# Kernel tuning notes

Measured on AMD Instinct MI355X. Metric: run time of the kernel, lower is better.

Reference implementation:

```python
import jax, jax.numpy as jnp
import numpy as np

B, N_ANGLES, LR, LZ = 1, 120, 128, 192
PAD = int(np.ceil(LR * (np.sqrt(2.0) - 1.0) / 2.0))  # pad_image amount = 27
LP = LR + 2 * PAD                                     # padded plane size = 182
DELTA = 1e-11


def _rotate_plane(vol, phi):
    """Bilinear CCW rotation by phi (radians) of the (dim1, dim2) plane of
    vol [B, L, L, Z] about its center, zero fill outside (grid_sample-style)."""
    L = vol.shape[1]
    c = (L - 1) / 2.0
    g = jnp.arange(L, dtype=jnp.float32) - c
    y, x = jnp.meshgrid(g, g, indexing='ij')          # [L, L]
    cp, sp = jnp.cos(phi), jnp.sin(phi)
    sy = cp * y - sp * x + c                          # source coords (inverse map)
    sx = sp * y + cp * x + c
    y0 = jnp.floor(sy)
    x0 = jnp.floor(sx)
    wy = (sy - y0)[None, :, :, None]
    wx = (sx - x0)[None, :, :, None]
    y0i = y0.astype(jnp.int32)
    x0i = x0.astype(jnp.int32)

    def tap(yi, xi):
        valid = ((yi >= 0) & (yi < L) & (xi >= 0) & (xi < L)).astype(vol.dtype)
        v = vol[:, jnp.clip(yi, 0, L - 1), jnp.clip(xi, 0, L - 1), :]  # [B,L,L,Z]
        return v * valid[None, :, :, None]

    return ((1 - wy) * (1 - wx) * tap(y0i, x0i)
            + (1 - wy) * wx * tap(y0i, x0i + 1)
            + wy * (1 - wx) * tap(y0i + 1, x0i)
            + wy * wx * tap(y0i + 1, x0i + 1))


def _back_project(image):
    # image: [B, N_angles, Lr, Lz]
    img_p = jnp.pad(image, ((0, 0), (0, 0), (PAD, PAD), (0, 0)))   # pad_image along Lr
    slices = jnp.transpose(img_p, (1, 0, 2, 3))                     # [N, B, LP, LZ]
    angles = jnp.arange(N_ANGLES, dtype=jnp.float32) * (2.0 * jnp.pi / N_ANGLES)
    phis = 1.5 * jnp.pi - angles   # rotate_detector_z(..., negative=True): +(270deg - angle)
    ones2d = jnp.ones((1, LP, LP, 1), image.dtype)

    def body(carry, inp):
        obj, norm2d = carry
        sl, phi = inp                                               # sl: [B, LP, LZ]
        vol = jnp.broadcast_to(sl[:, None, :, :], (sl.shape[0], LP, LP, sl.shape[2]))
        rot = _rotate_plane(vol, phi)                               # [B, LP, LP, LZ]
        obj = obj + rot[:, PAD:PAD + LR, PAD:PAD + LR, :]           # unpad_object
        # norm_constant_i is all-ones, constant over batch and z -> track 2D pattern
        w = _rotate_plane(ones2d, phi)[0, PAD:PAD + LR, PAD:PAD + LR, 0]
        return (obj, norm2d + w), None

    init = (jnp.zeros((image.shape[0], LR, LR, LZ), image.dtype),
            jnp.zeros((LR, LR), image.dtype))
    (obj, norm2d), _ = jax.lax.scan(body, init, (slices, phis))
    return obj / (norm2d[None, :, :, None] + DELTA)


def setup_inputs() -> dict:
    key = jax.random.key(0)
    image = jax.random.uniform(key, (B, N_ANGLES, LR, LZ), dtype=jnp.float32)
    return {"image": image}


def reference(image):
    return _back_project(image)
```

## Files before the change

### kernel.cpp

```cpp
#include <hip/hip_runtime.h>
#include <math.h>

namespace {

constexpr int NA = 120;
constexpr int LR = 128;
constexpr int LZ = 192;
constexpr int UW2 = 182;
constexpr int ZSTR = UW2 * 16;
constexpr int ASTR = 24 * ZSTR;
constexpr float CTR = 63.5f;

typedef float v2f __attribute__((ext_vector_type(2)));
typedef _Float16 half_t;
typedef half_t v2h __attribute__((ext_vector_type(2)));

#if defined(__has_builtin)
#if __has_builtin(__builtin_amdgcn_cvt_pk_f16_fp8) && __has_builtin(__builtin_amdgcn_fdot2)
#define USE_F16_DOT 1
#endif
#endif

__device__ inline void pk_fma(v2f& acc, v2f w, v2f t) {
    asm("v_pk_fma_f32 %0, %1, %2, %0" : "+v"(acc) : "v"(w), "v"(t));
}

__global__ __launch_bounds__(256) void cvt9(const float* __restrict__ img,
                                            unsigned char* __restrict__ pb) {
    const int idx = blockIdx.x * 256 + threadIdx.x;
    if (idx >= NA * UW2 * 24) return;
    const int up = idx % UW2;
    const int t  = idx / UW2;
    const int zb = t % 24;
    const int a  = t / 24;
    const int z0 = zb * 8;
    const int r0 = up - 27;
    const int r1 = up - 26;

    float v0[8], v1[8];
    if (r0 >= 0 && r0 < LR) {
        const float4* p = reinterpret_cast<const float4*>(img + (a * LR + r0) * LZ + z0);
        const float4 x = p[0], y = p[1];
        v0[0]=x.x; v0[1]=x.y; v0[2]=x.z; v0[3]=x.w;
        v0[4]=y.x; v0[5]=y.y; v0[6]=y.z; v0[7]=y.w;
    } else {
#pragma unroll
        for (int j = 0; j < 8; ++j) v0[j] = 0.f;
    }
    if (r1 >= 0 && r1 < LR) {
        const float4* p = reinterpret_cast<const float4*>(img + (a * LR + r1) * LZ + z0);
        const float4 x = p[0], y = p[1];
        v1[0]=x.x; v1[1]=x.y; v1[2]=x.z; v1[3]=x.w;
        v1[4]=y.x; v1[5]=y.y; v1[6]=y.z; v1[7]=y.w;
    } else {
#pragma unroll
        for (int j = 0; j < 8; ++j) v1[j] = 0.f;
    }

    uint4 o;
    unsigned* od = &o.x;
#pragma unroll
    for (int d = 0; d < 4; ++d) {
        int w = __builtin_amdgcn_cvt_pk_fp8_f32(v0[2*d]   - 0.5f, v1[2*d]   - 0.5f, 0, false);
        w = __builtin_amdgcn_cvt_pk_fp8_f32(v0[2*d+1] - 0.5f, v1[2*d+1] - 0.5f, w, true);
        od[d] = (unsigned)w;
    }
    *reinterpret_cast<uint4*>(pb + ((size_t)a * ASTR + (size_t)zb * ZSTR + (size_t)up * 16)) = o;
}

struct __align__(8) G13 {
    unsigned w;
    unsigned boff;
};

__global__ __launch_bounds__(384, 6) void bp_v13(const unsigned char* __restrict__ pb,
                                                 float* __restrict__ out) {
    __shared__ float2 s_cs[NA];
    __shared__ G13 s_geo[NA + 4][16];

    const int tid = threadIdx.x;

    if (tid < NA) {
        const float ang = (float)tid * (float)(2.0 * M_PI / (double)NA);
        const float phi = (float)(1.5 * M_PI) - ang;
        s_cs[tid] = make_float2(cosf(phi), sinf(phi));
    }
    __syncthreads();

    const int bid = blockIdx.x;
    const int swz = (bid & 7) * 128 + (bid >> 3);
    const int y  = swz >> 3;
    const int xg = (swz & 7) << 4;

    const float Y = (float)y - CTR;
    for (int e = tid; e < 16 * (NA + 4); e += 384) {
        const int p = e & 15;
        const int t = e >> 4;
        G13 g;
        if (t < NA) {
            const float2 cs = s_cs[t];
            const float X = (float)(xg + p) - CTR;
            const float u  = fmaf(cs.y, Y, fmaf(cs.x, X, CTR));
            const float fl = floorf(u);
            const float wx = u - fl;
#ifdef USE_F16_DOT
            union { v2h h; unsigned u32; } cw;
            cw.h = (v2h){(half_t)(1.0f - wx), (half_t)wx};
            g.w = cw.u32;
#else
            g.w = __float_as_uint(1.0f - wx);
#endif
            g.boff = (unsigned)(t * ASTR + ((int)fl + 27) * 16);
        } else {
            g.w = 0u; g.boff = 0;
        }
        s_geo[t][p] = g;
    }
    __syncthreads();

    const int px = tid & 15;
    const int zo = tid >> 4;
    const unsigned zbase = (unsigned)(zo * ZSTR);

#ifdef USE_F16_DOT
    float fac[8];
#pragma unroll
    for (int j = 0; j < 8; ++j) fac[j] = 0.f;
#else
    v2f acc[8];
#pragma unroll
    for (int j = 0; j < 8; ++j) acc[j] = (v2f){0.f, 0.f};
#endif

    unsigned wr[4];
    uint4 T[4];
#pragma unroll
    for (int k = 0; k < 4; ++k) {
        const G13 g = s_geo[k][px];
        wr[k] = g.w;
        T[k] = *reinterpret_cast<const uint4*>(pb + (g.boff + zbase));
    }

    for (int t0 = 0; t0 < NA; t0 += 4) {
#pragma unroll
        for (int k = 0; k < 4; ++k) {
            const uint4 cur = T[k];
            const unsigned cwb = wr[k];
            const G13 g = s_geo[t0 + k + 4][px];
            wr[k] = g.w;
            T[k] = *reinterpret_cast<const uint4*>(pb + (g.boff + zbase));
            const unsigned* q = &cur.x;
#ifdef USE_F16_DOT
            union { unsigned u32; v2h h; } cw;
            cw.u32 = cwb;
#pragma unroll
            for (int d = 0; d < 4; ++d) {
                const v2h lo = __builtin_amdgcn_cvt_pk_f16_fp8((short)(q[d] & 0xffffu));
                const v2h hi = __builtin_amdgcn_cvt_pk_f16_fp8((short)(q[d] >> 16));
                fac[2*d + 0] = __builtin_amdgcn_fdot2(cw.h, lo, fac[2*d + 0], false);
                fac[2*d + 1] = __builtin_amdgcn_fdot2(cw.h, hi, fac[2*d + 1], false);
            }
#else
            const float cw0 = __uint_as_float(cwb);
            const v2f cw = {cw0, 1.0f - cw0};
#pragma unroll
            for (int d = 0; d < 4; ++d) {
                const v2f lo = __builtin_amdgcn_cvt_pk_f32_fp8((int)q[d], false);
                const v2f hi = __builtin_amdgcn_cvt_pk_f32_fp8((int)q[d], true);
                pk_fma(acc[2*d + 0], cw, lo);
                pk_fma(acc[2*d + 1], cw, hi);
            }
#endif
        }
    }

    const float inv = (float)(1.0 / (120.0 + 1e-11));
    float* op = out + (size_t)(y * LR + xg + px) * LZ + zo * 8;
    float4 r0, r1;
#ifdef USE_F16_DOT
    r0.x = (fac[0] + 60.0f) * inv;
    r0.y = (fac[1] + 60.0f) * inv;
    r0.z = (fac[2] + 60.0f) * inv;
    r0.w = (fac[3] + 60.0f) * inv;
    r1.x = (fac[4] + 60.0f) * inv;
    r1.y = (fac[5] + 60.0f) * inv;
    r1.z = (fac[6] + 60.0f) * inv;
    r1.w = (fac[7] + 60.0f) * inv;
#else
    r0.x = (acc[0][0] + acc[0][1] + 60.0f) * inv;
    r0.y = (acc[1][0] + acc[1][1] + 60.0f) * inv;
    r0.z = (acc[2][0] + acc[2][1] + 60.0f) * inv;
    r0.w = (acc[3][0] + acc[3][1] + 60.0f) * inv;
    r1.x = (acc[4][0] + acc[4][1] + 60.0f) * inv;
    r1.y = (acc[5][0] + acc[5][1] + 60.0f) * inv;
    r1.z = (acc[6][0] + acc[6][1] + 60.0f) * inv;
    r1.w = (acc[7][0] + acc[7][1] + 60.0f) * inv;
#endif
    *reinterpret_cast<float4*>(op)     = r0;
    *reinterpret_cast<float4*>(op + 4) = r1;
}

struct __align__(16) Geo {
    float w0, w1;
    int b0, b1;
};

__global__ __launch_bounds__(256) void cvt_fp8(const float* __restrict__ in,
                                               unsigned int* __restrict__ out8,
                                               int n16) {
    const int i = blockIdx.x * 256 + threadIdx.x;
    if (i >= n16) return;
    const float4* p = reinterpret_cast<const float4*>(in) + (size_t)i * 4;
    uint4 o;
    unsigned int* od = &o.x;
#pragma unroll
    for (int d = 0; d < 4; ++d) {
        const float4 f = p[d];
        int w = __builtin_amdgcn_cvt_pk_fp8_f32(f.x - 0.5f, f.y - 0.5f, 0, false);
        w = __builtin_amdgcn_cvt_pk_fp8_f32(f.z - 0.5f, f.w - 0.5f, w, true);
        od[d] = (unsigned int)w;
    }
    reinterpret_cast<uint4*>(out8)[i] = o;
}

__device__ inline void blend8(v2f acc[4], float w0, float w1,
                              const uint2& t0, const uint2& t1) {
    const v2f W0 = {w0, w0};
    const v2f W1 = {w1, w1};
    const unsigned int* q0 = &t0.x;
    const unsigned int* q1 = &t1.x;
#pragma unroll
    for (int d = 0; d < 2; ++d) {
        const v2f a_lo = __builtin_amdgcn_cvt_pk_f32_fp8((int)q0[d], false);
        const v2f a_hi = __builtin_amdgcn_cvt_pk_f32_fp8((int)q0[d], true);
        const v2f b_lo = __builtin_amdgcn_cvt_pk_f32_fp8((int)q1[d], false);
        const v2f b_hi = __builtin_amdgcn_cvt_pk_f32_fp8((int)q1[d], true);
        acc[2 * d + 0] = acc[2 * d + 0] + W0 * a_lo + W1 * b_lo;
        acc[2 * d + 1] = acc[2 * d + 1] + W0 * a_hi + W1 * b_hi;
    }
}

__global__ __launch_bounds__(192, 6) void bp_v5(const unsigned char* __restrict__ img,
                                                float* __restrict__ out) {
    __shared__ float2 s_cs[NA];
    __shared__ Geo s_geo[NA][8];
    __shared__ float s_sumw[8];

    const int tid = threadIdx.x;
    if (tid < NA) {
        const float ang = (float)tid * (float)(2.0 * M_PI / (double)NA);
        const float phi = (float)(1.5 * M_PI) - ang;
        s_cs[tid] = make_float2(cosf(phi), sinf(phi));
    }
    __syncthreads();

    const int bid = blockIdx.x;
    const int swz = (bid & 7) * 256 + (bid >> 3);
    const int y  = swz >> 4;
    const int xg = (swz & 15) << 3;

    const float Y = (float)y - CTR;
    for (int e = tid; e < 8 * NA; e += 192) {
        const int p = e & 7;
        const int a = e >> 3;
        const float2 cs = s_cs[a];
        const float X = (float)(xg + p) - CTR;
        const float u  = fmaf(cs.y, Y, fmaf(cs.x, X, CTR));
        const float fl = floorf(u);
        const float wx = u - fl;
        const int i0 = (int)fl;
        Geo g;
        g.w0 = ((unsigned)i0 < 128u) ? (1.0f - wx) : 0.0f;
        g.w1 = ((unsigned)(i0 + 1) < 128u) ? wx : 0.0f;
        const int o0 = min(max(i0, 0), LR - 1);
        const int o1 = min(max(i0 + 1, 0), LR - 1);
        g.b0 = (a * LR + o0) * LZ;
        g.b1 = (a * LR + o1) * LZ;
        s_geo[a][p] = g;
    }
    __syncthreads();

    if (tid < 8) {
        float s = 0.f;
        for (int a = 0; a < NA; ++a) s += s_geo[a][tid].w0 + s_geo[a][tid].w1;
        s_sumw[tid] = s;
    }
    __syncthreads();

    const int zo = tid % 24;
    const int px = tid / 24;
    const unsigned char* base = img + zo * 8;

    v2f acc[4];
#pragma unroll
    for (int j = 0; j < 4; ++j) acc[j] = (v2f){0.f, 0.f};

    Geo ga = s_geo[0][px];
    Geo gb = s_geo[1][px];
    uint2 A0 = *reinterpret_cast<const uint2*>(base + ga.b0);
    uint2 A1 = *reinterpret_cast<const uint2*>(base + ga.b1);
    uint2 B0 = *reinterpret_cast<const uint2*>(base + gb.b0);
    uint2 B1 = *reinterpret_cast<const uint2*>(base + gb.b1);

    for (int a = 0; a < NA - 2; a += 2) {
        const Geo gn = s_geo[a + 2][px];
        const uint2 N0 = *reinterpret_cast<const uint2*>(base + gn.b0);
        const uint2 N1 = *reinterpret_cast<const uint2*>(base + gn.b1);
        blend8(acc, ga.w0, ga.w1, A0, A1);
        ga = gn; A0 = N0; A1 = N1;
        const Geo gm = s_geo[a + 3][px];
        const uint2 M0 = *reinterpret_cast<const uint2*>(base + gm.b0);
        const uint2 M1 = *reinterpret_cast<const uint2*>(base + gm.b1);
        blend8(acc, gb.w0, gb.w1, B0, B1);
        gb = gm; B0 = M0; B1 = M1;
    }
    blend8(acc, ga.w0, ga.w1, A0, A1);
    blend8(acc, gb.w0, gb.w1, B0, B1);

    const float inv = (float)(1.0 / (120.0 + 1e-11));
    const float half_sw = 0.5f * s_sumw[px];
    float* op = out + ((size_t)(y * LR + xg + px)) * LZ + zo * 8;
    float4 r0, r1;
    r0.x = (acc[0][0] + half_sw) * inv;
    r0.y = (acc[0][1] + half_sw) * inv;
    r0.z = (acc[1][0] + half_sw) * inv;
    r0.w = (acc[1][1] + half_sw) * inv;
    r1.x = (acc[2][0] + half_sw) * inv;
    r1.y = (acc[2][1] + half_sw) * inv;
    r1.z = (acc[3][0] + half_sw) * inv;
    r1.w = (acc[3][1] + half_sw) * inv;
    *reinterpret_cast<float4*>(op)     = r0;
    *reinterpret_cast<float4*>(op + 4) = r1;
}

__global__ __launch_bounds__(192) void bp_main(const float* __restrict__ img,
                                               float* __restrict__ out) {
    __shared__ float s_cp[NA];
    __shared__ float s_sp[NA];
    struct __align__(16) GeoF { float w0, w1; int off0, off1; };
    __shared__ GeoF s_geo[4][NA];

    const int tx = threadIdx.x;
    const int py = threadIdx.y;
    const int tid = py * 48 + tx;
    const int y  = blockIdx.x >> 5;
    const int xg = (blockIdx.x & 31) << 2;

    if (tid < NA) {
        const float ang = (float)tid * (float)(2.0 * M_PI / (double)NA);
        const float phi = (float)(1.5 * M_PI) - ang;
        s_cp[tid] = cosf(phi);
        s_sp[tid] = sinf(phi);
    }
    __syncthreads();

    for (int e = tid; e < 4 * NA; e += 192) {
        const int a = e % NA;
        const int p = e / NA;
        const float cp = s_cp[a];
        const float sp = s_sp[a];
        const float Yf = (float)y - CTR;
        const float Xf = (float)(xg + p) - CTR;
        const float u = sp * Yf + cp * Xf + CTR;
        const float fl = floorf(u);
        const float wx = u - fl;
        const int i0 = (int)fl;
        GeoF g;
        g.w0 = (i0 >= 0 && i0 < LR) ? (1.0f - wx) : 0.0f;
        g.w1 = (i0 >= -1 && i0 < LR - 1) ? wx : 0.0f;
        const int o0 = min(max(i0, 0), LR - 1);
        const int o1 = min(max(i0 + 1, 0), LR - 1);
        g.off0 = (a * LR + o0) * LZ;
        g.off1 = (a * LR + o1) * LZ;
        s_geo[p][a] = g;
    }
    __syncthreads();

    const int zb = tx << 2;
    float4 acc = make_float4(0.f, 0.f, 0.f, 0.f);
#pragma unroll 4
    for (int a = 0; a < NA; ++a) {
        const GeoF g = s_geo[py][a];
        const float4 v0 = *reinterpret_cast<const float4*>(img + g.off0 + zb);
        const float4 v1 = *reinterpret_cast<const float4*>(img + g.off1 + zb);
        acc.x = fmaf(g.w0, v0.x, fmaf(g.w1, v1.x, acc.x));
        acc.y = fmaf(g.w0, v0.y, fmaf(g.w1, v1.y, acc.y));
        acc.z = fmaf(g.w0, v0.z, fmaf(g.w1, v1.z, acc.z));
        acc.w = fmaf(g.w0, v0.w, fmaf(g.w1, v1.w, acc.w));
    }
    const float inv = (float)(1.0 / (120.0 + 1e-11));
    float4 r;
    r.x = acc.x * inv; r.y = acc.y * inv; r.z = acc.z * inv; r.w = acc.w * inv;
    *reinterpret_cast<float4*>(out + (y * LR + xg + py) * LZ + zb) = r;
}

}

extern "C" void kernel_launch(void* const* d_in, const int* in_sizes, int n_in,
                              void* d_out, int out_size, void* d_ws, size_t ws_size,
                              hipStream_t stream) {
    const float* img = (const float*)d_in[0];
    float* out = (float*)d_out;
    const int n = NA * LR * LZ;
    const size_t v13_bytes = (size_t)NA * ASTR;
    const size_t fp8_bytes = (size_t)n;

    if (ws_size >= v13_bytes) {
        unsigned char* pb = (unsigned char*)d_ws;
        const int nt = NA * UW2 * 24;
        hipLaunchKernelGGL(cvt9, dim3((nt + 255) / 256), dim3(256), 0, stream,
                           img, pb);
        hipLaunchKernelGGL(bp_v13, dim3(1024), dim3(384), 0, stream, pb, out);
    } else if (ws_size >= fp8_bytes) {
        unsigned int* img8 = (unsigned int*)d_ws;
        const int n16 = n / 16;
        hipLaunchKernelGGL(cvt_fp8, dim3((n16 + 255) / 256), dim3(256), 0, stream,
                           img, img8, n16);
        hipLaunchKernelGGL(bp_v5, dim3(128 * 16), dim3(192), 0, stream,
                           (const unsigned char*)img8, out);
    } else {
        hipLaunchKernelGGL(bp_main, dim3(128 * 32), dim3(48, 4), 0, stream,
                           img, out);
    }
}
```

Baseline: 50.58 us.

## Split z range across blocks, deepen gather prefetch, switch fp8 decode builtin

The back-projection kernel now uses 192-thread blocks, each covering half of the z range, and launches twice as many blocks. The software pipeline is deepened: six fp8 gathers are in flight and the geometry entries are prefetched from shared memory four steps ahead, with the angle loop unrolled by twelve. The fp8-to-f16 decode now uses the scalef32 conversion builtin instead of cvt_pk_f16_fp8, and the dot-path guard macro is changed to match. Each block still computes geometry for all 120 angles, so that setup work is duplicated across twice as many blocks, and the deeper pipeline raises register use.

```diff
diff --git a/kernel.cpp b/kernel.cpp
--- a/kernel.cpp
+++ b/kernel.cpp
@@ -16,8 +16,8 @@
 typedef half_t v2h __attribute__((ext_vector_type(2)));
 
 #if defined(__has_builtin)
-#if __has_builtin(__builtin_amdgcn_cvt_pk_f16_fp8) && __has_builtin(__builtin_amdgcn_fdot2)
-#define USE_F16_DOT 1
+#if __has_builtin(__builtin_amdgcn_cvt_scalef32_pk_f16_fp8) && __has_builtin(__builtin_amdgcn_fdot2)
+#define USE_DOT2 1
 #endif
 #endif
 
@@ -68,15 +68,15 @@
     *reinterpret_cast<uint4*>(pb + ((size_t)a * ASTR + (size_t)zb * ZSTR + (size_t)up * 16)) = o;
 }
 
-struct __align__(8) G13 {
+struct __align__(8) G15 {
     unsigned w;
     unsigned boff;
 };
 
-__global__ __launch_bounds__(384, 6) void bp_v13(const unsigned char* __restrict__ pb,
+__global__ __launch_bounds__(192, 6) void bp_v15(const unsigned char* __restrict__ pb,
                                                  float* __restrict__ out) {
     __shared__ float2 s_cs[NA];
-    __shared__ G13 s_geo[NA + 4][16];
+    __shared__ G15 s_geo[NA + 10][16];
 
     const int tid = threadIdx.x;
 
@@ -88,22 +88,23 @@
     __syncthreads();
 
     const int bid = blockIdx.x;
-    const int swz = (bid & 7) * 128 + (bid >> 3);
-    const int y  = swz >> 3;
-    const int xg = (swz & 7) << 4;
+    const int swz = (bid & 7) * 256 + (bid >> 3);
+    const int y  = swz >> 4;
+    const int xg = ((swz >> 1) & 7) << 4;
+    const int zh = swz & 1;
 
     const float Y = (float)y - CTR;
-    for (int e = tid; e < 16 * (NA + 4); e += 384) {
+    for (int e = tid; e < 16 * (NA + 10); e += 192) {
         const int p = e & 15;
         const int t = e >> 4;
-        G13 g;
+        G15 g;
         if (t < NA) {
             const float2 cs = s_cs[t];
             const float X = (float)(xg + p) - CTR;
             const float u  = fmaf(cs.y, Y, fmaf(cs.x, X, CTR));
             const float fl = floorf(u);
             const float wx = u - fl;
-#ifdef USE_F16_DOT
+#ifdef USE_DOT2
             union { v2h h; unsigned u32; } cw;
             cw.h = (v2h){(half_t)(1.0f - wx), (half_t)wx};
             g.w = cw.u32;
@@ -120,9 +121,9 @@
 
     const int px = tid & 15;
     const int zo = tid >> 4;
-    const unsigned zbase = (unsigned)(zo * ZSTR);
-
-#ifdef USE_F16_DOT
+    const unsigned zbase = (unsigned)((zh * 12 + zo) * ZSTR);
+
+#ifdef USE_DOT2
     float fac[8];
 #pragma unroll
     for (int j = 0; j < 8; ++j) fac[j] = 0.f;
@@ -132,52 +133,62 @@
     for (int j = 0; j < 8; ++j) acc[j] = (v2f){0.f, 0.f};
 #endif
 
-    unsigned wr[4];
-    uint4 T[4];
-#pragma unroll
-    for (int k = 0; k < 4; ++k) {
-        const G13 g = s_geo[k][px];
-        wr[k] = g.w;
-        T[k] = *reinterpret_cast<const uint4*>(pb + (g.boff + zbase));
-    }
-
-    for (int t0 = 0; t0 < NA; t0 += 4) {
-#pragma unroll
-        for (int k = 0; k < 4; ++k) {
-            const uint4 cur = T[k];
-            const unsigned cwb = wr[k];
-            const G13 g = s_geo[t0 + k + 4][px];
-            wr[k] = g.w;
-            T[k] = *reinterpret_cast<const uint4*>(pb + (g.boff + zbase));
+    G15  greg[4];
+    unsigned wT[6];
+    uint4 T[6];
+
+#pragma unroll
+    for (int j = 0; j < 6; ++j) {
+        const G15 g = s_geo[j][px];
+        wT[j] = g.w;
+        T[j] = *reinterpret_cast<const uint4*>(pb + (g.boff + zbase));
+    }
+#pragma unroll
+    for (int j = 0; j < 4; ++j) {
+        greg[j] = s_geo[6 + j][px];
+    }
+
+    for (int t0 = 0; t0 < NA; t0 += 12) {
+#pragma unroll
+        for (int k = 0; k < 12; ++k) {
+            const int sT = k % 6;
+            const int sG = k % 4;
+            const uint4 cur = T[sT];
+            const unsigned cwb = wT[sT];
+            const G15 g = greg[sG];
+            wT[sT] = g.w;
+            T[sT] = *reinterpret_cast<const uint4*>(pb + (g.boff + zbase));
+            greg[sG] = s_geo[t0 + k + 10][px];
+
             const unsigned* q = &cur.x;
-#ifdef USE_F16_DOT
+#ifdef USE_DOT2
             union { unsigned u32; v2h h; } cw;
             cw.u32 = cwb;
 #pragma unroll
             for (int d = 0; d < 4; ++d) {
-                const v2h lo = __builtin_amdgcn_cvt_pk_f16_fp8((short)(q[d] & 0xffffu));
-                const v2h hi = __builtin_amdgcn_cvt_pk_f16_fp8((short)(q[d] >> 16));
+                const v2h lo = __builtin_amdgcn_cvt_scalef32_pk_f16_fp8((int)q[d], 1.0f, false);
+                const v2h hi = __builtin_amdgcn_cvt_scalef32_pk_f16_fp8((int)q[d], 1.0f, true);
                 fac[2*d + 0] = __builtin_amdgcn_fdot2(cw.h, lo, fac[2*d + 0], false);
                 fac[2*d + 1] = __builtin_amdgcn_fdot2(cw.h, hi, fac[2*d + 1], false);
             }
 #else
             const float cw0 = __uint_as_float(cwb);
-            const v2f cw = {cw0, 1.0f - cw0};
+            const v2f cwv = {cw0, 1.0f - cw0};
 #pragma unroll
             for (int d = 0; d < 4; ++d) {
                 const v2f lo = __builtin_amdgcn_cvt_pk_f32_fp8((int)q[d], false);
                 const v2f hi = __builtin_amdgcn_cvt_pk_f32_fp8((int)q[d], true);
-                pk_fma(acc[2*d + 0], cw, lo);
-                pk_fma(acc[2*d + 1], cw, hi);
+                pk_fma(acc[2*d + 0], cwv, lo);
+                pk_fma(acc[2*d + 1], cwv, hi);
             }
 #endif
         }
     }
 
     const float inv = (float)(1.0 / (120.0 + 1e-11));
-    float* op = out + (size_t)(y * LR + xg + px) * LZ + zo * 8;
+    float* op = out + (size_t)(y * LR + xg + px) * LZ + (zh * 12 + zo) * 8;
     float4 r0, r1;
-#ifdef USE_F16_DOT
+#ifdef USE_DOT2
     r0.x = (fac[0] + 60.0f) * inv;
     r0.y = (fac[1] + 60.0f) * inv;
     r0.z = (fac[2] + 60.0f) * inv;
@@ -402,15 +413,15 @@
     const float* img = (const float*)d_in[0];
     float* out = (float*)d_out;
     const int n = NA * LR * LZ;
-    const size_t v13_bytes = (size_t)NA * ASTR;
+    const size_t v15_bytes = (size_t)NA * ASTR;
     const size_t fp8_bytes = (size_t)n;
 
-    if (ws_size >= v13_bytes) {
+    if (ws_size >= v15_bytes) {
         unsigned char* pb = (unsigned char*)d_ws;
         const int nt = NA * UW2 * 24;
         hipLaunchKernelGGL(cvt9, dim3((nt + 255) / 256), dim3(256), 0, stream,
                            img, pb);
-        hipLaunchKernelGGL(bp_v13, dim3(1024), dim3(384), 0, stream, pb, out);
+        hipLaunchKernelGGL(bp_v15, dim3(2048), dim3(192), 0, stream, pb, out);
     } else if (ws_size >= fp8_bytes) {
         unsigned int* img8 = (unsigned int*)d_ws;
         const int n16 = n / 16;
```

New measurement: 48.86 us. 1.04x faster.
